# Kernel tuning notes

Measured on AMD Instinct MI355X. Metric: run time of the kernel, lower is better.

Reference implementation:

```python
import jax, jax.numpy as jnp
import numpy as np

# module hyper-parameters (init_kwargs)
DELTA_VAR = 0.75
DELTA_DIST = 2.0
ALPHA, BETA, GAMMA = 1.0, 1.0, 0.001

B, E, H, W, C = 4, 16, 512, 512, 24


def _safe_norm(x, axis):
    # L2 norm with zero (not nan) gradient at 0, matching torch.norm's subgradient
    sq = jnp.sum(x * x, axis=axis)
    safe = jnp.where(sq == 0, 1.0, sq)
    return jnp.where(sq == 0, 0.0, jnp.sqrt(safe))


def setup_inputs() -> dict:
    key = jax.random.key(0)
    k1, k2 = jax.random.split(key)
    input_ = jax.random.normal(k1, (B, E, H, W), dtype=jnp.float32)
    target = jax.random.randint(k2, (B, 1, H, W), 0, C)  # consecutive labels 0..C-1 (w.h.p. all present)
    return {"input_": input_, "target": target, "n_instances": C}


def reference(input_, target, n_instances):
    # Discriminative loss (De Brabandere et al. 2017), math identical to the torch
    # one-hot-expansion version but expressed as segment reductions + gathers.
    Cn = int(n_instances)
    b, e = input_.shape[0], input_.shape[1]
    emb = input_.reshape(b, e, -1).transpose(0, 2, 1)  # (B, N, E)
    tgt = target.reshape(b, -1)                        # (B, N) int labels

    # per-instance cluster means: segment-sum over pixels (the torch code does the
    # same reduction via a dense BxCxExHxW one-hot expansion)
    def _means(e_bn, t_n):
        sums = jax.ops.segment_sum(e_bn, t_n, num_segments=Cn)                      # (C, E)
        counts = jax.ops.segment_sum(jnp.ones(t_n.shape, e_bn.dtype), t_n, num_segments=Cn)  # (C,)
        return sums / counts[:, None], counts

    mu, counts = jax.vmap(_means)(emb, tgt)            # (B, C, E), (B, C)

    # variance term: hinged distance of each pixel embedding to its own cluster mean
    mu_per_pix = jnp.take_along_axis(mu, tgt[:, :, None], axis=1)  # (B, N, E)
    dist = _safe_norm(emb - mu_per_pix, axis=-1)                   # (B, N)
    hinge = jnp.square(jnp.maximum(dist - DELTA_VAR, 0.0))
    var_per_inst = jax.vmap(lambda h, t: jax.ops.segment_sum(h, t, num_segments=Cn))(hinge, tgt) / counts  # (B, C)
    variance_term = jnp.mean(jnp.sum(var_per_inst, axis=1) / Cn)

    # distance term: hinged pairwise repulsion between cluster means
    dmat = _safe_norm(mu[:, :, None, :] - mu[:, None, :, :], axis=-1)  # (B, C, C)
    repulsion = 2.0 * DELTA_DIST * (1.0 - jnp.eye(Cn, dtype=mu.dtype))
    hinged = jnp.square(jnp.maximum(repulsion - dmat, 0.0))
    distance_term = jnp.mean(jnp.sum(hinged, axis=(1, 2))) / (Cn * (Cn - 1))

    # regularizer: mean norm of cluster means
    reg_term = jnp.mean(jnp.sum(_safe_norm(mu, axis=-1), axis=1)) / Cn

    return ALPHA * variance_term + BETA * distance_term + GAMMA * reg_term
```

## Files before the change

kernel.cpp:

```cpp
#include <hip/hip_runtime.h>
#include <cstdint>

#define B_SZ   4
#define E_DIM  16
#define C_INST 24
#define HW_N   262144
#define NG     (HW_N / 4)

#define DELTA_VAR  0.75f
#define DELTA_DIST 2.0f
#define ALPHA_W 1.0f
#define BETA_W  1.0f
#define GAMMA_W 0.001f

#define P1_NB   16
#define P1_ITER (NG / (P1_NB * 256))
#define ROW_STRIDE 51

__global__ __launch_bounds__(256) void pass1_kernel(
    const float* __restrict__ input, const int* __restrict__ target,
    float* __restrict__ sums, float* __restrict__ counts)
{
    __shared__ float buk[256][ROW_STRIDE];
    __shared__ float crow[4][C_INST];
    const int tid  = threadIdx.x;
    const int lane = tid & 63;
    const int wv   = tid >> 6;
    const int chunk = blockIdx.x;
    const int eg2   = blockIdx.y;
    const int b     = blockIdx.z;

    float* __restrict__ myrow = &buk[tid][0];
    #pragma unroll
    for (int j = 0; j < 2 * C_INST; ++j) myrow[j] = 0.f;

    const int4* __restrict__ tgt4 = (const int4*)(target + (size_t)b * HW_N);
    const float4* __restrict__ s0 =
        (const float4*)(input + ((size_t)b * E_DIM + 2 * eg2) * HW_N);
    const float4* __restrict__ s1 =
        (const float4*)(input + ((size_t)b * E_DIM + 2 * eg2 + 1) * HW_N);
    const int gbase = chunk * 256 * P1_ITER + tid;

    int scnt[C_INST];
    #pragma unroll
    for (int c = 0; c < C_INST; ++c) scnt[c] = 0;

    int4   lab = tgt4[gbase];
    float4 xa  = s0[gbase];
    float4 xb  = s1[gbase];
    #pragma unroll
    for (int it = 0; it < P1_ITER; ++it) {
        const int4   lc  = lab;
        const float4 xa0 = xa;
        const float4 xb0 = xb;
        if (it + 1 < P1_ITER) {
            lab = tgt4[gbase + (it + 1) * 256];
            xa  = s0[gbase + (it + 1) * 256];
            xb  = s1[gbase + (it + 1) * 256];
        }
        myrow[2 * lc.x]     += xa0.x;
        myrow[2 * lc.x + 1] += xb0.x;
        myrow[2 * lc.y]     += xa0.y;
        myrow[2 * lc.y + 1] += xb0.y;
        myrow[2 * lc.z]     += xa0.z;
        myrow[2 * lc.z + 1] += xb0.z;
        myrow[2 * lc.w]     += xa0.w;
        myrow[2 * lc.w + 1] += xb0.w;

        if ((it >> 1) == eg2) {
            #pragma unroll
            for (int c = 0; c < C_INST; ++c) {
                scnt[c] += (int)__popcll(__ballot(lc.x == c))
                         + (int)__popcll(__ballot(lc.y == c))
                         + (int)__popcll(__ballot(lc.z == c))
                         + (int)__popcll(__ballot(lc.w == c));
            }
        }
    }
    if (lane == 0) {
        #pragma unroll
        for (int c = 0; c < C_INST; ++c) crow[wv][c] = (float)scnt[c];
    }
    __syncthreads();

    if (tid < 4 * 2 * C_INST) {
        const int j  = tid >> 2;
        const int r0 = tid & 3;
        float s = 0.f;
        #pragma unroll
        for (int i = 0; i < 64; ++i) s += buk[4 * i + r0][j];
        s += __shfl_xor(s, 1, 64);
        s += __shfl_xor(s, 2, 64);
        if (r0 == 0) {
            const int c = j >> 1, d = j & 1;
            unsafeAtomicAdd(&sums[((size_t)b * E_DIM + 2 * eg2 + d) * C_INST + c], s);
        }
    }
    if (tid < C_INST) {
        const float s = crow[0][tid] + crow[1][tid] + crow[2][tid] + crow[3][tid];
        unsafeAtomicAdd(&counts[b * C_INST + tid], s);
    }
}

__global__ __launch_bounds__(256) void pass2_kernel(
    const float* __restrict__ input, const int* __restrict__ target,
    const float* __restrict__ sums, const float* __restrict__ counts,
    float* __restrict__ loss_acc)
{
    __shared__ float mu_l[C_INST][20];
    __shared__ float w_l[C_INST];
    __shared__ float redw[4];
    const int tid  = threadIdx.x;
    const int lane = tid & 63;
    const int wv   = tid >> 6;
    const int b    = blockIdx.y;

    if (tid < C_INST) {
        const float cv = counts[b * C_INST + tid];
        w_l[tid] = (cv > 0.f) ? 1.f / cv : 0.f;
    }
    __syncthreads();
    for (int i = tid; i < E_DIM * C_INST; i += 256) {
        const int e = i / C_INST, c = i % C_INST;
        mu_l[c][e] = sums[((size_t)b * E_DIM + e) * C_INST + c] * w_l[c];
    }
    __syncthreads();

    const int g = blockIdx.x * 256 + tid;
    const int4 lab4 = ((const int4*)(target + (size_t)b * HW_N))[g];
    const int lp[4] = {lab4.x, lab4.y, lab4.z, lab4.w};

    const float4* __restrict__ src4 = (const float4*)(input + (size_t)b * E_DIM * HW_N);
    float xs[E_DIM * 4];
    #pragma unroll
    for (int e = 0; e < E_DIM; ++e)
        ((float4*)xs)[e] = src4[(size_t)e * NG + g];

    float vloc = 0.f;
    #pragma unroll
    for (int p = 0; p < 4; ++p) {
        const int c = lp[p];
        float d2 = 0.f;
        #pragma unroll
        for (int e = 0; e < E_DIM; ++e) {
            const float df = xs[e * 4 + p] - mu_l[c][e];
            d2 = fmaf(df, df, d2);
        }
        const float h = fmaxf(sqrtf(d2) - DELTA_VAR, 0.f);
        vloc = fmaf(h * h, w_l[c], vloc);
    }

    #pragma unroll
    for (int m = 1; m < 64; m <<= 1) vloc += __shfl_xor(vloc, m, 64);
    if (lane == 0) redw[wv] = vloc;
    __syncthreads();
    if (tid == 0)
        unsafeAtomicAdd(loss_acc, redw[0] + redw[1] + redw[2] + redw[3]);
}

__global__ __launch_bounds__(256) void final_kernel(
    const float* __restrict__ sums, const float* __restrict__ counts,
    const float* __restrict__ loss_acc, float* __restrict__ out)
{
    __shared__ float mu[B_SZ][C_INST][E_DIM];
    __shared__ float red[256];
    const int tid = threadIdx.x;

    for (int i = tid; i < B_SZ * C_INST * E_DIM; i += 256) {
        const int b = i / (C_INST * E_DIM);
        const int r = i % (C_INST * E_DIM);
        const int e = r / C_INST, c = r % C_INST;
        const float cv = counts[b * C_INST + c];
        mu[b][c][e] = (cv > 0.f)
            ? sums[((size_t)b * E_DIM + e) * C_INST + c] / cv : 0.f;
    }
    __syncthreads();

    float acc = 0.f;
    for (int i = tid; i < B_SZ * C_INST; i += 256) {
        const int b = i / C_INST, c = i % C_INST;
        float n2 = 0.f;
        #pragma unroll
        for (int e = 0; e < E_DIM; ++e) n2 += mu[b][c][e] * mu[b][c][e];
        acc += GAMMA_W * sqrtf(n2) * (1.0f / (B_SZ * C_INST));
    }
    for (int i = tid; i < B_SZ * C_INST * C_INST; i += 256) {
        const int b  = i / (C_INST * C_INST);
        const int r  = i % (C_INST * C_INST);
        const int c1 = r / C_INST, c2 = r % C_INST;
        if (c1 != c2) {
            float d2 = 0.f;
            #pragma unroll
            for (int e = 0; e < E_DIM; ++e) {
                const float d = mu[b][c1][e] - mu[b][c2][e];
                d2 += d * d;
            }
            const float h = fmaxf(2.0f * DELTA_DIST - sqrtf(d2), 0.f);
            acc += BETA_W * h * h * (1.0f / (B_SZ * C_INST * (C_INST - 1)));
        }
    }

    red[tid] = acc;
    __syncthreads();
    for (int s = 128; s > 0; s >>= 1) {
        if (tid < s) red[tid] += red[tid + s];
        __syncthreads();
    }
    if (tid == 0)
        out[0] = red[0] + ALPHA_W * loss_acc[0] * (1.0f / (B_SZ * C_INST));
}

extern "C" void kernel_launch(void* const* d_in, const int* in_sizes, int n_in,
                              void* d_out, int out_size, void* d_ws, size_t ws_size,
                              hipStream_t stream)
{
    const float* input  = (const float*)d_in[0];
    const int*   target = (const int*)d_in[1];

    float* sums     = (float*)d_ws;
    float* counts   = sums + B_SZ * E_DIM * C_INST;
    float* loss_acc = counts + B_SZ * C_INST;
    const size_t ws_bytes =
        (size_t)(B_SZ * E_DIM * C_INST + B_SZ * C_INST + 1) * sizeof(float);
    hipMemsetAsync(d_ws, 0, ws_bytes, stream);

    pass1_kernel<<<dim3(P1_NB, E_DIM / 2, B_SZ), 256, 0, stream>>>(input, target, sums, counts);
    pass2_kernel<<<dim3(NG / 256, B_SZ), 256, 0, stream>>>(input, target, sums, counts, loss_acc);
    final_kernel<<<1, 256, 0, stream>>>(sums, counts, loss_acc, (float*)d_out);
}
```

Measured before the change: 133.6 us.

## Fold final reduction into pass2 via last-block flag, one channel per pass1 block

Pass1 now gives each block one embedding channel instead of two. That halves the shared-memory bucket rows and doubles the grid, so occupancy should rise. Pass2 loads its inputs in two batches of 8 channels to reduce register pressure. The separate final kernel is removed: the last pass2 block, found with an atomic counter and a threadfence, computes the distance and regularizer terms. This saves one kernel launch but adds an atomic per block and a serial tail on the last block.

```diff
diff --git a/kernel.cpp b/kernel.cpp
--- a/kernel.cpp
+++ b/kernel.cpp
@@ -15,30 +15,28 @@
 
 #define P1_NB   16
 #define P1_ITER (NG / (P1_NB * 256))
-#define ROW_STRIDE 51
+#define P2_TOTAL_BLOCKS (256 * B_SZ)
 
 __global__ __launch_bounds__(256) void pass1_kernel(
     const float* __restrict__ input, const int* __restrict__ target,
     float* __restrict__ sums, float* __restrict__ counts)
 {
-    __shared__ float buk[256][ROW_STRIDE];
+    __shared__ float buk[256][25];
     __shared__ float crow[4][C_INST];
     const int tid  = threadIdx.x;
     const int lane = tid & 63;
     const int wv   = tid >> 6;
     const int chunk = blockIdx.x;
-    const int eg2   = blockIdx.y;
+    const int eg    = blockIdx.y;
     const int b     = blockIdx.z;
 
     float* __restrict__ myrow = &buk[tid][0];
     #pragma unroll
-    for (int j = 0; j < 2 * C_INST; ++j) myrow[j] = 0.f;
+    for (int j = 0; j < C_INST; ++j) myrow[j] = 0.f;
 
     const int4* __restrict__ tgt4 = (const int4*)(target + (size_t)b * HW_N);
-    const float4* __restrict__ s0 =
-        (const float4*)(input + ((size_t)b * E_DIM + 2 * eg2) * HW_N);
-    const float4* __restrict__ s1 =
-        (const float4*)(input + ((size_t)b * E_DIM + 2 * eg2 + 1) * HW_N);
+    const float4* __restrict__ src4 =
+        (const float4*)(input + ((size_t)b * E_DIM + eg) * HW_N);
     const int gbase = chunk * 256 * P1_ITER + tid;
 
     int scnt[C_INST];
@@ -46,28 +44,20 @@
     for (int c = 0; c < C_INST; ++c) scnt[c] = 0;
 
     int4   lab = tgt4[gbase];
-    float4 xa  = s0[gbase];
-    float4 xb  = s1[gbase];
+    float4 x   = src4[gbase];
     #pragma unroll
     for (int it = 0; it < P1_ITER; ++it) {
-        const int4   lc  = lab;
-        const float4 xa0 = xa;
-        const float4 xb0 = xb;
+        const int4   lc = lab;
+        const float4 xc = x;
         if (it + 1 < P1_ITER) {
             lab = tgt4[gbase + (it + 1) * 256];
-            xa  = s0[gbase + (it + 1) * 256];
-            xb  = s1[gbase + (it + 1) * 256];
-        }
-        myrow[2 * lc.x]     += xa0.x;
-        myrow[2 * lc.x + 1] += xb0.x;
-        myrow[2 * lc.y]     += xa0.y;
-        myrow[2 * lc.y + 1] += xb0.y;
-        myrow[2 * lc.z]     += xa0.z;
-        myrow[2 * lc.z + 1] += xb0.z;
-        myrow[2 * lc.w]     += xa0.w;
-        myrow[2 * lc.w + 1] += xb0.w;
-
-        if ((it >> 1) == eg2) {
+            x   = src4[gbase + (it + 1) * 256];
+        }
+        myrow[lc.x] += xc.x;
+        myrow[lc.y] += xc.y;
+        myrow[lc.z] += xc.z;
+        myrow[lc.w] += xc.w;
+        if (it == eg) {
             #pragma unroll
             for (int c = 0; c < C_INST; ++c) {
                 scnt[c] += (int)__popcll(__ballot(lc.x == c))
@@ -83,18 +73,17 @@
     }
     __syncthreads();
 
-    if (tid < 4 * 2 * C_INST) {
-        const int j  = tid >> 2;
-        const int r0 = tid & 3;
+    if (tid < 8 * C_INST) {
+        const int c  = tid >> 3;
+        const int r0 = tid & 7;
         float s = 0.f;
         #pragma unroll
-        for (int i = 0; i < 64; ++i) s += buk[4 * i + r0][j];
+        for (int i = 0; i < 32; ++i) s += buk[8 * i + r0][c];
         s += __shfl_xor(s, 1, 64);
         s += __shfl_xor(s, 2, 64);
-        if (r0 == 0) {
-            const int c = j >> 1, d = j & 1;
-            unsafeAtomicAdd(&sums[((size_t)b * E_DIM + 2 * eg2 + d) * C_INST + c], s);
-        }
+        s += __shfl_xor(s, 4, 64);
+        if (r0 == 0)
+            unsafeAtomicAdd(&sums[((size_t)b * E_DIM + eg) * C_INST + c], s);
     }
     if (tid < C_INST) {
         const float s = crow[0][tid] + crow[1][tid] + crow[2][tid] + crow[3][tid];
@@ -105,11 +94,13 @@
 __global__ __launch_bounds__(256) void pass2_kernel(
     const float* __restrict__ input, const int* __restrict__ target,
     const float* __restrict__ sums, const float* __restrict__ counts,
-    float* __restrict__ loss_acc)
+    float* __restrict__ loss_acc, unsigned int* __restrict__ done,
+    float* __restrict__ out)
 {
-    __shared__ float mu_l[C_INST][20];
+    __shared__ float mu_l[C_INST][17];
     __shared__ float w_l[C_INST];
     __shared__ float redw[4];
+    __shared__ int lastf;
     const int tid  = threadIdx.x;
     const int lane = tid & 63;
     const int wv   = tid >> 6;
@@ -128,86 +119,97 @@
 
     const int g = blockIdx.x * 256 + tid;
     const int4 lab4 = ((const int4*)(target + (size_t)b * HW_N))[g];
-    const int lp[4] = {lab4.x, lab4.y, lab4.z, lab4.w};
-
-    const float4* __restrict__ src4 = (const float4*)(input + (size_t)b * E_DIM * HW_N);
-    float xs[E_DIM * 4];
-    #pragma unroll
-    for (int e = 0; e < E_DIM; ++e)
-        ((float4*)xs)[e] = src4[(size_t)e * NG + g];
+    const float4* __restrict__ src4 =
+        (const float4*)(input + (size_t)b * E_DIM * HW_N);
+
+    float d2[4] = {0.f, 0.f, 0.f, 0.f};
+    #pragma unroll
+    for (int e8 = 0; e8 < 2; ++e8) {
+        float4 xv[8];
+        #pragma unroll
+        for (int e = 0; e < 8; ++e)
+            xv[e] = src4[(size_t)(e8 * 8 + e) * NG + g];
+        #pragma unroll
+        for (int e = 0; e < 8; ++e) {
+            const int ee = e8 * 8 + e;
+            float df;
+            df = xv[e].x - mu_l[lab4.x][ee]; d2[0] = fmaf(df, df, d2[0]);
+            df = xv[e].y - mu_l[lab4.y][ee]; d2[1] = fmaf(df, df, d2[1]);
+            df = xv[e].z - mu_l[lab4.z][ee]; d2[2] = fmaf(df, df, d2[2]);
+            df = xv[e].w - mu_l[lab4.w][ee]; d2[3] = fmaf(df, df, d2[3]);
+        }
+    }
 
     float vloc = 0.f;
-    #pragma unroll
-    for (int p = 0; p < 4; ++p) {
-        const int c = lp[p];
-        float d2 = 0.f;
-        #pragma unroll
-        for (int e = 0; e < E_DIM; ++e) {
-            const float df = xs[e * 4 + p] - mu_l[c][e];
-            d2 = fmaf(df, df, d2);
-        }
-        const float h = fmaxf(sqrtf(d2) - DELTA_VAR, 0.f);
-        vloc = fmaf(h * h, w_l[c], vloc);
-    }
-
+    {
+        const int lp[4] = {lab4.x, lab4.y, lab4.z, lab4.w};
+        #pragma unroll
+        for (int p = 0; p < 4; ++p) {
+            const float h = fmaxf(sqrtf(d2[p]) - DELTA_VAR, 0.f);
+            vloc = fmaf(h * h, w_l[lp[p]], vloc);
+        }
+    }
     #pragma unroll
     for (int m = 1; m < 64; m <<= 1) vloc += __shfl_xor(vloc, m, 64);
     if (lane == 0) redw[wv] = vloc;
     __syncthreads();
-    if (tid == 0)
+
+    if (tid == 0) {
         unsafeAtomicAdd(loss_acc, redw[0] + redw[1] + redw[2] + redw[3]);
-}
-
-__global__ __launch_bounds__(256) void final_kernel(
-    const float* __restrict__ sums, const float* __restrict__ counts,
-    const float* __restrict__ loss_acc, float* __restrict__ out)
-{
-    __shared__ float mu[B_SZ][C_INST][E_DIM];
-    __shared__ float red[256];
-    const int tid = threadIdx.x;
-
-    for (int i = tid; i < B_SZ * C_INST * E_DIM; i += 256) {
-        const int b = i / (C_INST * E_DIM);
-        const int r = i % (C_INST * E_DIM);
-        const int e = r / C_INST, c = r % C_INST;
-        const float cv = counts[b * C_INST + c];
-        mu[b][c][e] = (cv > 0.f)
-            ? sums[((size_t)b * E_DIM + e) * C_INST + c] / cv : 0.f;
-    }
-    __syncthreads();
-
-    float acc = 0.f;
-    for (int i = tid; i < B_SZ * C_INST; i += 256) {
-        const int b = i / C_INST, c = i % C_INST;
-        float n2 = 0.f;
-        #pragma unroll
-        for (int e = 0; e < E_DIM; ++e) n2 += mu[b][c][e] * mu[b][c][e];
-        acc += GAMMA_W * sqrtf(n2) * (1.0f / (B_SZ * C_INST));
-    }
-    for (int i = tid; i < B_SZ * C_INST * C_INST; i += 256) {
-        const int b  = i / (C_INST * C_INST);
-        const int r  = i % (C_INST * C_INST);
-        const int c1 = r / C_INST, c2 = r % C_INST;
-        if (c1 != c2) {
-            float d2 = 0.f;
+        __threadfence();
+        const unsigned int t = atomicAdd(done, 1u);
+        lastf = (t == P2_TOTAL_BLOCKS - 1) ? 1 : 0;
+    }
+    __syncthreads();
+
+    if (lastf) {
+        __shared__ float mu3[B_SZ][C_INST][E_DIM];
+        __shared__ float red[256];
+        for (int i = tid; i < B_SZ * C_INST * E_DIM; i += 256) {
+            const int bb = i / (C_INST * E_DIM);
+            const int r  = i % (C_INST * E_DIM);
+            const int e  = r / C_INST, c = r % C_INST;
+            const float cv = counts[bb * C_INST + c];
+            mu3[bb][c][e] = (cv > 0.f)
+                ? sums[((size_t)bb * E_DIM + e) * C_INST + c] / cv : 0.f;
+        }
+        __syncthreads();
+
+        float acc = 0.f;
+        for (int i = tid; i < B_SZ * C_INST; i += 256) {
+            const int bb = i / C_INST, c = i % C_INST;
+            float n2 = 0.f;
             #pragma unroll
-            for (int e = 0; e < E_DIM; ++e) {
-                const float d = mu[b][c1][e] - mu[b][c2][e];
-                d2 += d * d;
+            for (int e = 0; e < E_DIM; ++e) n2 += mu3[bb][c][e] * mu3[bb][c][e];
+            acc += GAMMA_W * sqrtf(n2) * (1.0f / (B_SZ * C_INST));
+        }
+        for (int i = tid; i < B_SZ * C_INST * C_INST; i += 256) {
+            const int bb = i / (C_INST * C_INST);
+            const int r  = i % (C_INST * C_INST);
+            const int c1 = r / C_INST, c2 = r % C_INST;
+            if (c1 != c2) {
+                float dd2 = 0.f;
+                #pragma unroll
+                for (int e = 0; e < E_DIM; ++e) {
+                    const float d = mu3[bb][c1][e] - mu3[bb][c2][e];
+                    dd2 += d * d;
+                }
+                const float h = fmaxf(2.0f * DELTA_DIST - sqrtf(dd2), 0.f);
+                acc += BETA_W * h * h * (1.0f / (B_SZ * C_INST * (C_INST - 1)));
             }
-            const float h = fmaxf(2.0f * DELTA_DIST - sqrtf(d2), 0.f);
-            acc += BETA_W * h * h * (1.0f / (B_SZ * C_INST * (C_INST - 1)));
-        }
-    }
-
-    red[tid] = acc;
-    __syncthreads();
-    for (int s = 128; s > 0; s >>= 1) {
-        if (tid < s) red[tid] += red[tid + s];
+        }
+
+        red[tid] = acc;
         __syncthreads();
-    }
-    if (tid == 0)
-        out[0] = red[0] + ALPHA_W * loss_acc[0] * (1.0f / (B_SZ * C_INST));
+        for (int s = 128; s > 0; s >>= 1) {
+            if (tid < s) red[tid] += red[tid + s];
+            __syncthreads();
+        }
+        if (tid == 0) {
+            const float vsum = atomicAdd(loss_acc, 0.0f);
+            out[0] = red[0] + ALPHA_W * vsum * (1.0f / (B_SZ * C_INST));
+        }
+    }
 }
 
 extern "C" void kernel_launch(void* const* d_in, const int* in_sizes, int n_in,
@@ -220,11 +222,12 @@
     float* sums     = (float*)d_ws;
     float* counts   = sums + B_SZ * E_DIM * C_INST;
     float* loss_acc = counts + B_SZ * C_INST;
+    unsigned int* done = (unsigned int*)(loss_acc + 1);
     const size_t ws_bytes =
-        (size_t)(B_SZ * E_DIM * C_INST + B_SZ * C_INST + 1) * sizeof(float);
+        (size_t)(B_SZ * E_DIM * C_INST + B_SZ * C_INST + 2) * sizeof(float);
     hipMemsetAsync(d_ws, 0, ws_bytes, stream);
 
-    pass1_kernel<<<dim3(P1_NB, E_DIM / 2, B_SZ), 256, 0, stream>>>(input, target, sums, counts);
-    pass2_kernel<<<dim3(NG / 256, B_SZ), 256, 0, stream>>>(input, target, sums, counts, loss_acc);
-    final_kernel<<<1, 256, 0, stream>>>(sums, counts, loss_acc, (float*)d_out);
+    pass1_kernel<<<dim3(P1_NB, E_DIM, B_SZ), 256, 0, stream>>>(input, target, sums, counts);
+    pass2_kernel<<<dim3(256, B_SZ), 256, 0, stream>>>(input, target, sums, counts,
+                                                      loss_acc, done, (float*)d_out);
 }
```

Result: slower. 154.4 us (+15.5%).
